# Kernel optimization log

Measured on AMD Instinct MI355X. Metric: run time of the kernel, lower is better.

Reference implementation:

```python
import jax, jax.numpy as jnp
import numpy as np

N = 50000      # nodes
E = 800000     # edges
F_IN = 512     # input feature dim
H1 = 8         # heads layer 1
F_HID = 8      # per-head hidden dim (concat -> 64)
H2 = 1         # heads layer 2
NLAB = 64      # output classes
LRELU_SLOPE = 0.2


def setup_inputs() -> dict:
    key = jax.random.key(0)
    ks = jax.random.split(key, 9)
    inputs = jax.random.normal(ks[0], (N, F_IN), jnp.float32)
    src = jax.random.randint(ks[1], (E,), 0, N, dtype=jnp.int32)
    dst = jax.random.randint(ks[2], (E,), 0, N, dtype=jnp.int32)
    s1 = 1.0 / np.sqrt(F_IN)
    s2 = 1.0 / np.sqrt(H1 * F_HID)
    W1 = jax.random.normal(ks[3], (H1, F_IN, F_HID), jnp.float32) * s1
    a1_src = jax.random.normal(ks[4], (H1, F_HID), jnp.float32) * 0.1
    a1_dst = jax.random.normal(ks[5], (H1, F_HID), jnp.float32) * 0.1
    W2 = jax.random.normal(ks[6], (H2, H1 * F_HID, NLAB), jnp.float32) * s2
    a2_src = jax.random.normal(ks[7], (H2, NLAB), jnp.float32) * 0.1
    a2_dst = jax.random.normal(ks[8], (H2, NLAB), jnp.float32) * 0.1
    return {"inputs": inputs, "W1": W1, "a1_src": a1_src, "a1_dst": a1_dst,
            "W2": W2, "a2_src": a2_src, "a2_dst": a2_dst, "src": src, "dst": dst}


def gat_layer(x, W, a_s, a_d, src, dst):
    # x: [N, F]; W: [H, F, O]; a_s/a_d: [H, O]
    Wh = jnp.einsum('nf,hfo->nho', x, W)                    # [N, H, O]
    es = jnp.einsum('nho,ho->nh', Wh, a_s)                  # [N, H]
    ed = jnp.einsum('nho,ho->nh', Wh, a_d)                  # [N, H]
    e = jax.nn.leaky_relu(es[src] + ed[dst], LRELU_SLOPE)   # [E, H]
    # neighborhood softmax over incoming edges of each dst node
    m = jax.lax.stop_gradient(jax.ops.segment_max(e, dst, num_segments=N))
    ex = jnp.exp(e - m[dst])                                # [E, H]
    den = jax.ops.segment_sum(ex, dst, num_segments=N)      # [N, H]
    alpha = ex / (den[dst] + 1e-10)                         # [E, H]
    msgs = alpha[:, :, None] * Wh[src]                      # [E, H, O]
    return jax.ops.segment_sum(msgs, dst, num_segments=N)   # [N, H, O]


def reference(inputs, W1, a1_src, a1_dst, W2, a2_src, a2_dst, src, dst):
    # eval mode: dropout rate 0, identity
    h = gat_layer(inputs, W1, a1_src, a1_dst, src, dst)     # [N, H1, F_HID]
    h = jax.nn.elu(h.reshape(N, H1 * F_HID))                # concat heads (reduction=False)
    o = gat_layer(h, W2, a2_src, a2_dst, src, dst)          # [N, H2, NLAB]
    o = o.mean(axis=1)                                      # average heads (reduction=True)
    return jax.nn.softmax(o, axis=-1)                       # [N, NLAB] (squeezed)
```

## Files before the change

kernel.cpp:

```cpp
#include <hip/hip_runtime.h>
#include <math.h>

#define N_NODES 50000
#define N_EDGES 800000
#define F_IN    512
#define H1      8
#define F_HID   8
#define C1      64
#define NLAB    64
#define SLOPE   0.2f
#define MAXDEG  64

#define NBIN    98
#define BINCAP  9216
#define NBLK_WT  128
#define NBLK_E   196
#define NBLK_G1  782

typedef __attribute__((ext_vector_type(8))) short short8;
typedef __attribute__((ext_vector_type(4))) float f32x4;

__device__ __forceinline__ float bf_lo(unsigned u) { return __uint_as_float(u << 16); }
__device__ __forceinline__ float bf_hi(unsigned u) { return __uint_as_float(u & 0xFFFF0000u); }
__device__ __forceinline__ unsigned short f2bf(float x) {
    unsigned bits = __float_as_uint(x);
    return (unsigned short)((bits + 0x7FFF + ((bits >> 16) & 1)) >> 16);
}

__global__ void k_prep(const float* __restrict__ W1, unsigned short* __restrict__ Bh,
                       unsigned short* __restrict__ Bl,
                       const int* __restrict__ src, const int* __restrict__ dst,
                       int2* __restrict__ ebuf, int* __restrict__ gctr) {
    int b = blockIdx.x;
    if (b < NBLK_WT) {
        int i = b * 256 + threadIdx.x;
        int c = i >> 9, f = i & 511;
        float v = W1[(c >> 3) * (F_IN * F_HID) + f * F_HID + (c & 7)];
        unsigned bits = __float_as_uint(v);
        float r = v - __uint_as_float(bits & 0xFFFF0000u);
        Bh[i] = (unsigned short)(bits >> 16);
        Bl[i] = (unsigned short)(__float_as_uint(r) >> 16);
        return;
    }
    __shared__ int hist[NBIN];
    __shared__ int cur[NBIN];
    const int t = threadIdx.x;
    const int eb = b - NBLK_WT;
    if (t < NBIN) hist[t] = 0;
    __syncthreads();
    int4 dv[4], sv[4];
    const int e0 = eb * 4096 + t * 4;
    #pragma unroll
    for (int i = 0; i < 4; i++) {
        int e = e0 + i * 1024;
        if (e < N_EDGES) {
            dv[i] = *(const int4*)(dst + e);
            sv[i] = *(const int4*)(src + e);
            atomicAdd(&hist[dv[i].x >> 9], 1);
            atomicAdd(&hist[dv[i].y >> 9], 1);
            atomicAdd(&hist[dv[i].z >> 9], 1);
            atomicAdd(&hist[dv[i].w >> 9], 1);
        }
    }
    __syncthreads();
    if (t < NBIN) cur[t] = atomicAdd(&gctr[t], hist[t]);
    __syncthreads();
    #pragma unroll
    for (int i = 0; i < 4; i++) {
        int e = e0 + i * 1024;
        if (e < N_EDGES) {
            int d, s, sl;
            d = dv[i].x; s = sv[i].x; sl = atomicAdd(&cur[d >> 9], 1);
            ebuf[(size_t)(d >> 9) * BINCAP + min(sl, BINCAP - 1)] = make_int2(d, s);
            d = dv[i].y; s = sv[i].y; sl = atomicAdd(&cur[d >> 9], 1);
            ebuf[(size_t)(d >> 9) * BINCAP + min(sl, BINCAP - 1)] = make_int2(d, s);
            d = dv[i].z; s = sv[i].z; sl = atomicAdd(&cur[d >> 9], 1);
            ebuf[(size_t)(d >> 9) * BINCAP + min(sl, BINCAP - 1)] = make_int2(d, s);
            d = dv[i].w; s = sv[i].w; sl = atomicAdd(&cur[d >> 9], 1);
            ebuf[(size_t)(d >> 9) * BINCAP + min(sl, BINCAP - 1)] = make_int2(d, s);
        }
    }
}

__launch_bounds__(256)
__global__ void k_gemm1f(const float* __restrict__ X, const unsigned short* __restrict__ Bh,
                         const unsigned short* __restrict__ Bl, const float* __restrict__ a_s,
                         const float* __restrict__ a_d, float* __restrict__ es1,
                         unsigned short* __restrict__ wh1, float* __restrict__ ed,
                         const int2* __restrict__ ebuf, const int* __restrict__ gctr,
                         int* __restrict__ deg, int* __restrict__ colPad) {
    __shared__ unsigned short sBh[64][136];
    __shared__ unsigned short sBl[64][136];

    const int b = blockIdx.x;
    const int t = threadIdx.x;
    if (b < NBIN) {
        int* cnt = (int*)&sBh[0][0];
        const int lo = b << 9;
        const int cnum = min(gctr[b], BINCAP);
        for (int i = t; i < 512; i += 256) cnt[i] = 0;
        __syncthreads();
        const int2* eb2 = ebuf + (size_t)b * BINCAP;
        for (int i = t; i < cnum; i += 256) {
            int2 e = eb2[i];
            int sl = atomicAdd(&cnt[e.x - lo], 1);
            colPad[(e.x << 6) | min(sl, MAXDEG - 1)] = e.y;
        }
        __syncthreads();
        for (int i = t; i < 512; i += 256) {
            int n = lo + i;
            if (n < N_NODES) deg[n] = min(cnt[i], MAXDEG);
        }
        return;
    }

    const int lane = t & 63, w = t >> 6;
    const int r0 = (b - NBIN) * 64 + w * 16;
    const int m = lane & 15, quad = lane >> 4;
    int row = r0 + m; if (row >= N_NODES) row = N_NODES - 1;
    const float* xrow = X + (size_t)row * F_IN + quad * 8;

    const int sc = t >> 2;
    const int sp = t & 3;

    f32x4 acc[4] = {};
    float4 pxa[4], pxb[4];
    #pragma unroll
    for (int i = 0; i < 4; i++) {
        pxa[i] = *(const float4*)(xrow + i * 32);
        pxb[i] = *(const float4*)(xrow + i * 32 + 4);
    }

    for (int chunk = 0; chunk < 4; chunk++) {
        const int k0 = chunk * 128;
        if (chunk) __syncthreads();
        #pragma unroll
        for (int i = 0; i < 4; i++) {
            *(short8*)(&sBh[sc][sp * 32 + i * 8]) =
                *(const short8*)(Bh + sc * F_IN + k0 + sp * 32 + i * 8);
            *(short8*)(&sBl[sc][sp * 32 + i * 8]) =
                *(const short8*)(Bl + sc * F_IN + k0 + sp * 32 + i * 8);
        }
        __syncthreads();
        #pragma unroll
        for (int i = 0; i < 4; i++) {
            float xs[8] = {pxa[i].x, pxa[i].y, pxa[i].z, pxa[i].w,
                           pxb[i].x, pxb[i].y, pxb[i].z, pxb[i].w};
            if (chunk < 3) {
                const int ktn = k0 + 128 + i * 32;
                pxa[i] = *(const float4*)(xrow + ktn);
                pxb[i] = *(const float4*)(xrow + ktn + 4);
            }
            short8 ah, al;
            #pragma unroll
            for (int j = 0; j < 8; j++) {
                unsigned bits = __float_as_uint(xs[j]);
                float rr = xs[j] - __uint_as_float(bits & 0xFFFF0000u);
                ah[j] = (short)(bits >> 16);
                al[j] = (short)(__float_as_uint(rr) >> 16);
            }
            #pragma unroll
            for (int s = 0; s < 4; s++) {
                short8 bh = *(const short8*)(&sBh[s * 16 + m][i * 32 + quad * 8]);
                short8 bl = *(const short8*)(&sBl[s * 16 + m][i * 32 + quad * 8]);
                acc[s] = __builtin_amdgcn_mfma_f32_16x16x32_bf16(al, bh, acc[s], 0, 0, 0);
                acc[s] = __builtin_amdgcn_mfma_f32_16x16x32_bf16(ah, bl, acc[s], 0, 0, 0);
                acc[s] = __builtin_amdgcn_mfma_f32_16x16x32_bf16(ah, bh, acc[s], 0, 0, 0);
            }
        }
    }
    __syncthreads();
    unsigned short* sWh = &sBh[0][0] + w * 1024;
    #pragma unroll
    for (int s = 0; s < 4; s++)
        #pragma unroll
        for (int reg = 0; reg < 4; reg++)
            sWh[(quad * 4 + reg) * 64 + s * 16 + m] = f2bf(acc[s][reg]);
    __syncthreads();
    const int rr = lane & 15, p = lane >> 4;
    const int n = r0 + rr;
    if (n >= N_NODES) return;
    float es2v[2], edv[2];
    #pragma unroll
    for (int hh = 0; hh < 2; hh++) {
        int h = 2 * p + hh;
        float s = 0.f, dsum = 0.f;
        #pragma unroll
        for (int j = 0; j < 8; j++) {
            float v = __uint_as_float((unsigned)sWh[rr * 64 + h * 8 + j] << 16);
            s += v * a_s[h * 8 + j];
            dsum += v * a_d[h * 8 + j];
        }
        es2v[hh] = s; edv[hh] = dsum;
    }
    *(float2*)(es1 + n * 8 + 2 * p) = make_float2(es2v[0], es2v[1]);
    *(short8*)(wh1 + (size_t)n * 64 + p * 16)     = *(const short8*)(sWh + rr * 64 + p * 16);
    *(short8*)(wh1 + (size_t)n * 64 + p * 16 + 8) = *(const short8*)(sWh + rr * 64 + p * 16 + 8);
    *(float2*)(ed + n * 8 + 2 * p) = make_float2(edv[0], edv[1]);
}

__launch_bounds__(256)
__global__ void k_agg1g2(const float* __restrict__ es1, const unsigned short* __restrict__ wh1,
                         const float* __restrict__ ed,
                         const int* __restrict__ deg, const int* __restrict__ colPad,
                         const float* __restrict__ W2, const float* __restrict__ a2s,
                         const float* __restrict__ a2d,
                         float* __restrict__ es2, unsigned short* __restrict__ wh2,
                         float* __restrict__ ed2) {
    __shared__ float Ws[64 * 64];
    __shared__ float hs[32][64];
    const int t = threadIdx.x;
    #pragma unroll
    for (int i = 0; i < 4; i++) {
        int flat = i * 256 + t;
        *(float4*)(Ws + flat * 4) = *(const float4*)(W2 + flat * 4);
    }
    const int n0 = blockIdx.x * 32;
    const int n = n0 + (t >> 3), q = t & 7;
    const int gb = (t & 63) & 56;

    float o[8] = {};
    if (n < N_NODES) {
        const int d = deg[n];
        const int base = n << 6;
        int4 c0 = *(const int4*)(colPad + base + q * 4);
        int4 c1 = *(const int4*)(colPad + base + 32 + q * 4);
        float edq = ed[n * 8 + q];
        float den = 0.f;
        float acc[8] = {};
        #pragma unroll
        for (int comp = 0; comp < 4; comp++) {
            int m0 = (comp == 0) ? c0.x : (comp == 1) ? c0.y : (comp == 2) ? c0.z : c0.w;
            int m1 = (comp == 0) ? c1.x : (comp == 1) ? c1.y : (comp == 2) ? c1.z : c1.w;
            #pragma unroll
            for (int srcl = 0; srcl < 8; srcl++) {
                int sv0 = __shfl(m0, gb + srcl);
                int sv1 = __shfl(m1, gb + srcl);
                int i0 = srcl * 4 + comp;
                if (i0 < d) {
                    float x = es1[sv0 * 8 + q] + edq;
                    uint4 u = *(const uint4*)(wh1 + (size_t)sv0 * 64 + q * 8);
                    x = x > 0.f ? x : SLOPE * x;
                    float wg = __expf(x);
                    den += wg;
                    acc[0] += wg * bf_lo(u.x); acc[1] += wg * bf_hi(u.x);
                    acc[2] += wg * bf_lo(u.y); acc[3] += wg * bf_hi(u.y);
                    acc[4] += wg * bf_lo(u.z); acc[5] += wg * bf_hi(u.z);
                    acc[6] += wg * bf_lo(u.w); acc[7] += wg * bf_hi(u.w);
                }
                if (i0 + 32 < d) {
                    float x = es1[sv1 * 8 + q] + edq;
                    uint4 u = *(const uint4*)(wh1 + (size_t)sv1 * 64 + q * 8);
                    x = x > 0.f ? x : SLOPE * x;
                    float wg = __expf(x);
                    den += wg;
                    acc[0] += wg * bf_lo(u.x); acc[1] += wg * bf_hi(u.x);
                    acc[2] += wg * bf_lo(u.y); acc[3] += wg * bf_hi(u.y);
                    acc[4] += wg * bf_lo(u.z); acc[5] += wg * bf_hi(u.z);
                    acc[6] += wg * bf_lo(u.w); acc[7] += wg * bf_hi(u.w);
                }
            }
        }
        float inv = 1.f / (den + 1e-10f);
        #pragma unroll
        for (int j = 0; j < 8; j++) {
            float v = acc[j] * inv;
            o[j] = v > 0.f ? v : expm1f(v);
        }
    }
    float4* hp = (float4*)(&hs[t >> 3][q * 8]);
    hp[0] = make_float4(o[0], o[1], o[2], o[3]);
    hp[1] = make_float4(o[4], o[5], o[6], o[7]);
    __syncthreads();

    const int wv = t >> 6, lane = t & 63;
    float as = a2s[lane], ad = a2d[lane];
    #pragma unroll
    for (int j = 0; j < 8; j++) {
        int nl = wv * 8 + j;
        int nn = n0 + nl;
        if (nn >= N_NODES) break;
        float acc = 0.f;
        #pragma unroll
        for (int k = 0; k < 64; k++) acc += hs[nl][k] * Ws[k * 64 + lane];
        wh2[(size_t)nn * 64 + lane] = f2bf(acc);
        float s = acc * as;
        float dd = acc * ad;
        #pragma unroll
        for (int off = 1; off < 64; off <<= 1) {
            s += __shfl_xor(s, off);
            dd += __shfl_xor(dd, off);
        }
        if (lane == 0) { es2[nn] = s; ed2[nn] = dd; }
    }
}

__launch_bounds__(256)
__global__ void k_agg2(const float* __restrict__ es2, const unsigned short* __restrict__ wh2,
                       const float* __restrict__ ed2,
                       const int* __restrict__ deg, const int* __restrict__ colPad,
                       float* __restrict__ out) {
    int tid = blockIdx.x * 256 + threadIdx.x;
    int n = tid >> 3, q = tid & 7;
    if (n >= N_NODES) return;
    const int t = threadIdx.x;
    const int gb = (t & 63) & 56;
    const int d = deg[n];
    const int base = n << 6;
    int4 c0 = *(const int4*)(colPad + base + q * 4);
    int4 c1 = *(const int4*)(colPad + base + 32 + q * 4);
    float edn = ed2[n];

    float den = 0.f;
    float acc[8] = {};
    #pragma unroll
    for (int comp = 0; comp < 4; comp++) {
        int m0 = (comp == 0) ? c0.x : (comp == 1) ? c0.y : (comp == 2) ? c0.z : c0.w;
        int m1 = (comp == 0) ? c1.x : (comp == 1) ? c1.y : (comp == 2) ? c1.z : c1.w;
        #pragma unroll
        for (int srcl = 0; srcl < 8; srcl++) {
            int sv0 = __shfl(m0, gb + srcl);
            int sv1 = __shfl(m1, gb + srcl);
            int i0 = srcl * 4 + comp;
            if (i0 < d) {
                float x = es2[sv0] + edn;
                uint4 u = *(const uint4*)(wh2 + (size_t)sv0 * 64 + q * 8);
                x = x > 0.f ? x : SLOPE * x;
                float wg = __expf(x);
                den += wg;
                acc[0] += wg * bf_lo(u.x); acc[1] += wg * bf_hi(u.x);
                acc[2] += wg * bf_lo(u.y); acc[3] += wg * bf_hi(u.y);
                acc[4] += wg * bf_lo(u.z); acc[5] += wg * bf_hi(u.z);
                acc[6] += wg * bf_lo(u.w); acc[7] += wg * bf_hi(u.w);
            }
            if (i0 + 32 < d) {
                float x = es2[sv1] + edn;
                uint4 u = *(const uint4*)(wh2 + (size_t)sv1 * 64 + q * 8);
                x = x > 0.f ? x : SLOPE * x;
                float wg = __expf(x);
                den += wg;
                acc[0] += wg * bf_lo(u.x); acc[1] += wg * bf_hi(u.x);
                acc[2] += wg * bf_lo(u.y); acc[3] += wg * bf_hi(u.y);
                acc[4] += wg * bf_lo(u.z); acc[5] += wg * bf_hi(u.z);
                acc[6] += wg * bf_lo(u.w); acc[7] += wg * bf_hi(u.w);
            }
        }
    }
    float inv = 1.f / (den + 1e-10f);
    float o[8];
    #pragma unroll
    for (int j = 0; j < 8; j++) o[j] = acc[j] * inv;
    float mx = o[0];
    #pragma unroll
    for (int j = 1; j < 8; j++) mx = fmaxf(mx, o[j]);
    mx = fmaxf(mx, __shfl_xor(mx, 1));
    mx = fmaxf(mx, __shfl_xor(mx, 2));
    mx = fmaxf(mx, __shfl_xor(mx, 4));
    float e8[8], sm = 0.f;
    #pragma unroll
    for (int j = 0; j < 8; j++) { e8[j] = __expf(o[j] - mx); sm += e8[j]; }
    sm += __shfl_xor(sm, 1);
    sm += __shfl_xor(sm, 2);
    sm += __shfl_xor(sm, 4);
    float inv2 = 1.f / sm;
    float4* op = (float4*)(out + (size_t)n * 64 + q * 8);
    op[0] = make_float4(e8[0] * inv2, e8[1] * inv2, e8[2] * inv2, e8[3] * inv2);
    op[1] = make_float4(e8[4] * inv2, e8[5] * inv2, e8[6] * inv2, e8[7] * inv2);
}

extern "C" void kernel_launch(void* const* d_in, const int* in_sizes, int n_in,
                              void* d_out, int out_size, void* d_ws, size_t ws_size,
                              hipStream_t stream) {
    const float* X   = (const float*)d_in[0];
    const float* W1  = (const float*)d_in[1];
    const float* a1s = (const float*)d_in[2];
    const float* a1d = (const float*)d_in[3];
    const float* W2  = (const float*)d_in[4];
    const float* a2s = (const float*)d_in[5];
    const float* a2d = (const float*)d_in[6];
    const int*   src = (const int*)d_in[7];
    const int*   dst = (const int*)d_in[8];
    float* out = (float*)d_out;

    char* w = (char*)d_ws;
    size_t off = 0;
    auto alloc = [&](size_t bytes) {
        void* p = w + off;
        off += (bytes + 255) & ~(size_t)255;
        return p;
    };
    unsigned short* Bh   = (unsigned short*)alloc((size_t)C1 * F_IN * 2);
    unsigned short* Bl   = (unsigned short*)alloc((size_t)C1 * F_IN * 2);
    float*          es1  = (float*)alloc((size_t)N_NODES * 8 * 4);
    unsigned short* wh1  = (unsigned short*)alloc((size_t)N_NODES * 64 * 2);
    float*          es2  = (float*)alloc((size_t)N_NODES * 4);
    unsigned short* wh2  = (unsigned short*)alloc((size_t)N_NODES * 64 * 2);
    float*          ed1  = (float*)alloc((size_t)N_NODES * 8 * 4);
    float*          ed2  = (float*)alloc((size_t)N_NODES * 4);
    int*            deg  = (int*)alloc((size_t)N_NODES * 4);
    int*            colPad = (int*)alloc((size_t)N_NODES * MAXDEG * 4);
    int2*           ebuf = (int2*)alloc((size_t)NBIN * BINCAP * 8);
    int*            gctr = (int*)alloc((size_t)NBIN * 4);

    hipMemsetAsync(gctr, 0, NBIN * 4, stream);

    k_prep<<<NBLK_WT + NBLK_E, 256, 0, stream>>>(W1, Bh, Bl, src, dst, ebuf, gctr);
    k_gemm1f<<<NBIN + NBLK_G1, 256, 0, stream>>>(X, Bh, Bl, a1s, a1d, es1, wh1, ed1,
                                                 ebuf, gctr, deg, colPad);
    k_agg1g2<<<(N_NODES + 31) / 32, 256, 0, stream>>>(es1, wh1, ed1, deg, colPad,
                                                      W2, a2s, a2d, es2, wh2, ed2);
    k_agg2<<<(N_NODES * 8 + 255) / 256, 256, 0, stream>>>(es2, wh2, ed2, deg, colPad, out);
}
```

Measured before the change: 274.0 us.

## Overlap edge binning with layer-1 GEMM and split CSR build into own kernel

```diff
diff --git a/kernel.cpp b/kernel.cpp
--- a/kernel.cpp
+++ b/kernel.cpp
@@ -28,94 +28,70 @@
 }
 
 __global__ void k_prep(const float* __restrict__ W1, unsigned short* __restrict__ Bh,
-                       unsigned short* __restrict__ Bl,
-                       const int* __restrict__ src, const int* __restrict__ dst,
-                       int2* __restrict__ ebuf, int* __restrict__ gctr) {
-    int b = blockIdx.x;
-    if (b < NBLK_WT) {
-        int i = b * 256 + threadIdx.x;
-        int c = i >> 9, f = i & 511;
-        float v = W1[(c >> 3) * (F_IN * F_HID) + f * F_HID + (c & 7)];
-        unsigned bits = __float_as_uint(v);
-        float r = v - __uint_as_float(bits & 0xFFFF0000u);
-        Bh[i] = (unsigned short)(bits >> 16);
-        Bl[i] = (unsigned short)(__float_as_uint(r) >> 16);
-        return;
-    }
-    __shared__ int hist[NBIN];
-    __shared__ int cur[NBIN];
-    const int t = threadIdx.x;
-    const int eb = b - NBLK_WT;
-    if (t < NBIN) hist[t] = 0;
-    __syncthreads();
-    int4 dv[4], sv[4];
-    const int e0 = eb * 4096 + t * 4;
-    #pragma unroll
-    for (int i = 0; i < 4; i++) {
-        int e = e0 + i * 1024;
-        if (e < N_EDGES) {
-            dv[i] = *(const int4*)(dst + e);
-            sv[i] = *(const int4*)(src + e);
-            atomicAdd(&hist[dv[i].x >> 9], 1);
-            atomicAdd(&hist[dv[i].y >> 9], 1);
-            atomicAdd(&hist[dv[i].z >> 9], 1);
-            atomicAdd(&hist[dv[i].w >> 9], 1);
-        }
-    }
-    __syncthreads();
-    if (t < NBIN) cur[t] = atomicAdd(&gctr[t], hist[t]);
-    __syncthreads();
-    #pragma unroll
-    for (int i = 0; i < 4; i++) {
-        int e = e0 + i * 1024;
-        if (e < N_EDGES) {
-            int d, s, sl;
-            d = dv[i].x; s = sv[i].x; sl = atomicAdd(&cur[d >> 9], 1);
-            ebuf[(size_t)(d >> 9) * BINCAP + min(sl, BINCAP - 1)] = make_int2(d, s);
-            d = dv[i].y; s = sv[i].y; sl = atomicAdd(&cur[d >> 9], 1);
-            ebuf[(size_t)(d >> 9) * BINCAP + min(sl, BINCAP - 1)] = make_int2(d, s);
-            d = dv[i].z; s = sv[i].z; sl = atomicAdd(&cur[d >> 9], 1);
-            ebuf[(size_t)(d >> 9) * BINCAP + min(sl, BINCAP - 1)] = make_int2(d, s);
-            d = dv[i].w; s = sv[i].w; sl = atomicAdd(&cur[d >> 9], 1);
-            ebuf[(size_t)(d >> 9) * BINCAP + min(sl, BINCAP - 1)] = make_int2(d, s);
-        }
-    }
-}
-
-__launch_bounds__(256)
-__global__ void k_gemm1f(const float* __restrict__ X, const unsigned short* __restrict__ Bh,
+                       unsigned short* __restrict__ Bl) {
+    int i = blockIdx.x * 256 + threadIdx.x;
+    int c = i >> 9, f = i & 511;
+    float v = W1[(c >> 3) * (F_IN * F_HID) + f * F_HID + (c & 7)];
+    unsigned bits = __float_as_uint(v);
+    float r = v - __uint_as_float(bits & 0xFFFF0000u);
+    Bh[i] = (unsigned short)(bits >> 16);
+    Bl[i] = (unsigned short)(__float_as_uint(r) >> 16);
+}
+
+__launch_bounds__(256, 4)
+__global__ void k_gemm1b(const float* __restrict__ X, const unsigned short* __restrict__ Bh,
                          const unsigned short* __restrict__ Bl, const float* __restrict__ a_s,
                          const float* __restrict__ a_d, float* __restrict__ es1,
                          unsigned short* __restrict__ wh1, float* __restrict__ ed,
-                         const int2* __restrict__ ebuf, const int* __restrict__ gctr,
-                         int* __restrict__ deg, int* __restrict__ colPad) {
+                         const int* __restrict__ src, const int* __restrict__ dst,
+                         int2* __restrict__ ebuf, int* __restrict__ gctr) {
     __shared__ unsigned short sBh[64][136];
     __shared__ unsigned short sBl[64][136];
 
     const int b = blockIdx.x;
     const int t = threadIdx.x;
-    if (b < NBIN) {
-        int* cnt = (int*)&sBh[0][0];
-        const int lo = b << 9;
-        const int cnum = min(gctr[b], BINCAP);
-        for (int i = t; i < 512; i += 256) cnt[i] = 0;
+    if (b < NBLK_E) {
+        int* hist = (int*)&sBh[0][0];
+        int* cur  = hist + 128;
+        if (t < NBIN) hist[t] = 0;
         __syncthreads();
-        const int2* eb2 = ebuf + (size_t)b * BINCAP;
-        for (int i = t; i < cnum; i += 256) {
-            int2 e = eb2[i];
-            int sl = atomicAdd(&cnt[e.x - lo], 1);
-            colPad[(e.x << 6) | min(sl, MAXDEG - 1)] = e.y;
+        int4 dv[4], sv[4];
+        const int e0 = b * 4096 + t * 4;
+        #pragma unroll
+        for (int i = 0; i < 4; i++) {
+            int e = e0 + i * 1024;
+            if (e < N_EDGES) {
+                dv[i] = *(const int4*)(dst + e);
+                sv[i] = *(const int4*)(src + e);
+                atomicAdd(&hist[dv[i].x >> 9], 1);
+                atomicAdd(&hist[dv[i].y >> 9], 1);
+                atomicAdd(&hist[dv[i].z >> 9], 1);
+                atomicAdd(&hist[dv[i].w >> 9], 1);
+            }
         }
         __syncthreads();
-        for (int i = t; i < 512; i += 256) {
-            int n = lo + i;
-            if (n < N_NODES) deg[n] = min(cnt[i], MAXDEG);
+        if (t < NBIN) cur[t] = atomicAdd(&gctr[t], hist[t]);
+        __syncthreads();
+        #pragma unroll
+        for (int i = 0; i < 4; i++) {
+            int e = e0 + i * 1024;
+            if (e < N_EDGES) {
+                int d, s, sl;
+                d = dv[i].x; s = sv[i].x; sl = atomicAdd(&cur[d >> 9], 1);
+                ebuf[(size_t)(d >> 9) * BINCAP + min(sl, BINCAP - 1)] = make_int2(d, s);
+                d = dv[i].y; s = sv[i].y; sl = atomicAdd(&cur[d >> 9], 1);
+                ebuf[(size_t)(d >> 9) * BINCAP + min(sl, BINCAP - 1)] = make_int2(d, s);
+                d = dv[i].z; s = sv[i].z; sl = atomicAdd(&cur[d >> 9], 1);
+                ebuf[(size_t)(d >> 9) * BINCAP + min(sl, BINCAP - 1)] = make_int2(d, s);
+                d = dv[i].w; s = sv[i].w; sl = atomicAdd(&cur[d >> 9], 1);
+                ebuf[(size_t)(d >> 9) * BINCAP + min(sl, BINCAP - 1)] = make_int2(d, s);
+            }
         }
         return;
     }
 
     const int lane = t & 63, w = t >> 6;
-    const int r0 = (b - NBIN) * 64 + w * 16;
+    const int r0 = (b - NBLK_E) * 64 + w * 16;
     const int m = lane & 15, quad = lane >> 4;
     int row = r0 + m; if (row >= N_NODES) row = N_NODES - 1;
     const float* xrow = X + (size_t)row * F_IN + quad * 8;
@@ -197,6 +173,27 @@
     *(short8*)(wh1 + (size_t)n * 64 + p * 16)     = *(const short8*)(sWh + rr * 64 + p * 16);
     *(short8*)(wh1 + (size_t)n * 64 + p * 16 + 8) = *(const short8*)(sWh + rr * 64 + p * 16 + 8);
     *(float2*)(ed + n * 8 + 2 * p) = make_float2(edv[0], edv[1]);
+}
+
+__global__ void k_csr(const int2* __restrict__ ebuf, const int* __restrict__ gctr,
+                      int* __restrict__ deg, int* __restrict__ colPad) {
+    __shared__ int cnt[512];
+    const int b = blockIdx.x, t = threadIdx.x;
+    const int lo = b << 9;
+    const int cnum = min(gctr[b], BINCAP);
+    for (int i = t; i < 512; i += 256) cnt[i] = 0;
+    __syncthreads();
+    const int2* eb2 = ebuf + (size_t)b * BINCAP;
+    for (int i = t; i < cnum; i += 256) {
+        int2 e = eb2[i];
+        int sl = atomicAdd(&cnt[e.x - lo], 1);
+        colPad[(e.x << 6) | min(sl, MAXDEG - 1)] = e.y;
+    }
+    __syncthreads();
+    for (int i = t; i < 512; i += 256) {
+        int n = lo + i;
+        if (n < N_NODES) deg[n] = min(cnt[i], MAXDEG);
+    }
 }
 
 __launch_bounds__(256)
@@ -404,9 +401,10 @@
 
     hipMemsetAsync(gctr, 0, NBIN * 4, stream);
 
-    k_prep<<<NBLK_WT + NBLK_E, 256, 0, stream>>>(W1, Bh, Bl, src, dst, ebuf, gctr);
-    k_gemm1f<<<NBIN + NBLK_G1, 256, 0, stream>>>(X, Bh, Bl, a1s, a1d, es1, wh1, ed1,
-                                                 ebuf, gctr, deg, colPad);
+    k_prep<<<NBLK_WT, 256, 0, stream>>>(W1, Bh, Bl);
+    k_gemm1b<<<NBLK_E + NBLK_G1, 256, 0, stream>>>(X, Bh, Bl, a1s, a1d, es1, wh1, ed1,
+                                                   src, dst, ebuf, gctr);
+    k_csr<<<NBIN, 256, 0, stream>>>(ebuf, gctr, deg, colPad);
     k_agg1g2<<<(N_NODES + 31) / 32, 256, 0, stream>>>(es1, wh1, ed1, deg, colPad,
                                                       W2, a2s, a2d, es2, wh2, ed2);
     k_agg2<<<(N_NODES * 8 + 255) / 256, 256, 0, stream>>>(es2, wh2, ed2, deg, colPad, out);
```

Result: no change. 269.6 us (-1.6%).
